# Kernel tuning notes

Measured on AMD Instinct MI355X. Metric: run time of the kernel, lower is better.

## Reference

```python
import jax, jax.numpy as jnp
import numpy as np
from jax import lax

# 4D convolution: XLA's general conv supports 4 spatial dims directly.
# dim numbers: N C + 4 spatial (H1 W1 H2 W2)
_DN = ('NCHWDT', 'OIHWDT', 'NCHWDT')


def conv4d(x, w, b):
    # x: [B, Cin, H1, W1, H2, W2]; w: [Cout, Cin, 3,3,3,3]; b: [Cout]
    y = lax.conv_general_dilated(x, w, window_strides=(1, 1, 1, 1),
                                 padding=[(1, 1)] * 4,
                                 dimension_numbers=_DN)
    return y + b.reshape(1, -1, 1, 1, 1, 1)


def setup_inputs() -> dict:
    key = jax.random.key(0)
    ks = jax.random.split(key, 7)
    B, S = 2, 30
    x = jax.random.normal(ks[0], (B, 1, S, S, S, S), dtype=jnp.float32)
    # Conv4d weights, fan-in scaled (kernel 3^4 = 81)
    w1 = jax.random.normal(ks[1], (10, 1, 3, 3, 3, 3), dtype=jnp.float32) * (1.0 / np.sqrt(1 * 81))
    b1 = jax.random.normal(ks[2], (10,), dtype=jnp.float32) * 0.01
    w2 = jax.random.normal(ks[3], (10, 10, 3, 3, 3, 3), dtype=jnp.float32) * (1.0 / np.sqrt(10 * 81))
    b2 = jax.random.normal(ks[4], (10,), dtype=jnp.float32) * 0.01
    w3 = jax.random.normal(ks[5], (1, 10, 3, 3, 3, 3), dtype=jnp.float32) * (1.0 / np.sqrt(10 * 81))
    b3 = jax.random.normal(ks[6], (1,), dtype=jnp.float32) * 0.01
    return {"x": x, "w1": w1, "b1": b1, "w2": w2, "b2": b2, "w3": w3, "b3": b3}


def reference(x, w1, b1, w2, b2, w3, b3):
    def net(t):
        for w, b in ((w1, b1), (w2, b2), (w3, b3)):
            t = jax.nn.relu(conv4d(t, w, b))
        return t

    # symmetric mode: f(x) + permute(f(permute(x)))
    perm = (0, 1, 4, 5, 2, 3)
    return net(x) + jnp.transpose(net(jnp.transpose(x, perm)), perm)
```

## Files before the change

kernel.cpp:

```cpp
#include <hip/hip_runtime.h>


static constexpr int S  = 30;
static constexpr long S4 = 810000;
static constexpr size_t PLANE = 32768;
static constexpr size_t YBYTES = (size_t)1800 * PLANE;

typedef __bf16 bf16x8 __attribute__((ext_vector_type(8)));
typedef float  f32x16 __attribute__((ext_vector_type(16)));
typedef unsigned int  u32;
typedef unsigned short u16;

static __device__ __forceinline__ u16 f2bf(float f) {
    u32 u = __builtin_bit_cast(u32, f);
    return (u16)((u + 0x7fffu + ((u >> 16) & 1u)) >> 16);
}

__global__ __launch_bounds__(256) void fragprep_k(u32* __restrict__ ft,
    const float* __restrict__ w1, const float* __restrict__ w2,
    const float* __restrict__ w3)
{
    const int gid = blockIdx.x * 256 + threadIdx.x;
    if (gid >= 6 * 27 * 64) return;
    const int lane = gid & 63;
    int r = gid >> 6;
    const int k3 = r % 3; r /= 3;
    const int k12 = r % 9; const int set = r / 9;
    const int layer = set >> 1, swap = set & 1;
    const int k1 = k12 / 3, k2 = k12 % 3;
    const int n = lane & 31, hl = lane >> 5;

    u16 us[8];
#pragma unroll
    for (int j = 0; j < 8; ++j) us[j] = 0;
    if (n < 30) {
        const int k4 = (n < 10) ? 0 : ((n < 20) ? 1 : 2);
        const int co = n - 10 * k4;
        const int i1 = swap ? k3 : k1, i2 = swap ? k4 : k2;
        const int i3 = swap ? k1 : k3, i4 = swap ? k2 : k4;
        const int widx = ((i1 * 3 + i2) * 3 + i3) * 3 + i4;
#pragma unroll
        for (int j = 0; j < 8; ++j) {
            const int k = hl * 8 + j;
            float wv = 0.f;
            if (layer == 0) { if (k == 0) wv = w1[co * 81 + widx]; }
            else if (layer == 1) { if (k < 10) wv = w2[(co * 10 + k) * 81 + widx]; }
            else { if (k < 10 && co == 0) wv = w3[k * 81 + widx]; }
            us[j] = f2bf(wv);
        }
    }
    u32* o = ft + (size_t)gid * 4;
    o[0] = (u32)us[0] | ((u32)us[1] << 16);
    o[1] = (u32)us[2] | ((u32)us[3] << 16);
    o[2] = (u32)us[4] | ((u32)us[5] << 16);
    o[3] = (u32)us[6] | ((u32)us[7] << 16);
}

__global__ __launch_bounds__(128) void zerok(u16* __restrict__ y1, u16* __restrict__ y2)
{
    const int pb = blockIdx.x, tid = threadIdx.x;
    if (tid >= 124) return;
    int hp, tp;
    if (tid < 32)      { hp = 0;        tp = tid; }
    else if (tid < 64) { hp = 31;       tp = tid - 32; }
    else if (tid < 94) { hp = tid - 63; tp = 0; }
    else               { hp = tid - 93; tp = 31; }
    const size_t off = (size_t)pb * PLANE + hp * 1024 + tp * 32;
    const uint4 z = make_uint4(0, 0, 0, 0);
    *(uint4*)((char*)y1 + off)      = z;
    *(uint4*)((char*)y1 + off + 16) = z;
    *(uint4*)((char*)y2 + off)      = z;
    *(uint4*)((char*)y2 + off + 16) = z;
}

template<int LAYER, bool ACCUM>
__global__ __launch_bounds__(256, 2) void conv_k(
    const void* __restrict__ inp, const u32* __restrict__ ftab,
    const float* __restrict__ bias, void* __restrict__ outp)
{
    __shared__ float E[4][1056];
    const int wgid = blockIdx.x + S * blockIdx.y + 900 * blockIdx.z;
    const int id2  = (wgid & 7) * 450 + (wgid >> 3);
    const int half = id2 & 1;
    int sp = id2 >> 1;
    const int w1i = sp % S; sp /= S;
    const int h1  = sp % S;
    const int b   = sp / S;

    const int tid = threadIdx.x;
    const int lane = tid & 63, wv = tid >> 6;
    const int m = lane & 31, hl = lane >> 5;
    const int rbase = half * 15 + wv * 4;
    const uint4* ft4 = (const uint4*)ftab;

    int rofs[6];
#pragma unroll
    for (int f = 0; f < 6; ++f) {
        int rr = rbase + f; if (rr > 31) rr = 31;
        rofs[f] = rr * 1024;
    }

    int kl[9], nk = 0;
#pragma unroll
    for (int k12 = 0; k12 < 9; ++k12) {
        const int g1 = h1 + k12 / 3 - 1, g2 = w1i + k12 % 3 - 1;
        if (g1 >= 0 && g1 < S && g2 >= 0 && g2 < S)
            kl[nk++] = (g1 * S + g2) | (k12 << 10);
    }

    f32x16 acc[4];
#pragma unroll
    for (int r = 0; r < 4; ++r)
#pragma unroll
        for (int e = 0; e < 16; ++e) acc[r][e] = 0.f;

    auto loadA = [&](uint4* Fd, int g) {
        if (LAYER == 0) {
            const float* xp = (const float*)inp + ((size_t)b * 900 + g) * 900;
#pragma unroll
            for (int f = 0; f < 6; ++f) {
                const int hp = rbase + f;
                float v = 0.f;
                if (hl == 0 && hp >= 1 && hp <= 30 && m >= 1 && m <= 30)
                    v = xp[(hp - 1) * 30 + (m - 1)];
                Fd[f] = make_uint4((u32)f2bf(v), 0u, 0u, 0u);
            }
        } else {
            const char* P = (const char*)inp + ((size_t)b * 900 + g) * PLANE
                            + m * 32 + hl * 16;
#pragma unroll
            for (int f = 0; f < 6; ++f)
                Fd[f] = *(const uint4*)(P + rofs[f]);
        }
    };

    uint4 B0[3];
    {
        const int k0 = kl[0] >> 10;
#pragma unroll
        for (int f = 0; f < 3; ++f) B0[f] = ft4[(k0 * 3 + f) * 64 + lane];
    }
    uint4 F[6];
    loadA(F, kl[0] & 1023);

    for (int ki = 0; ki + 1 < nk; ++ki) {
        const int gn = kl[ki + 1] & 1023, kn = kl[ki + 1] >> 10;
        uint4 FN[6];
        loadA(FN, gn);
        uint4 BN[3];
#pragma unroll
        for (int f = 0; f < 3; ++f) BN[f] = ft4[(kn * 3 + f) * 64 + lane];

#pragma unroll
        for (int ss = 0; ss < 3; ++ss)
#pragma unroll
            for (int r = 0; r < 4; ++r)
                acc[r] = __builtin_amdgcn_mfma_f32_32x32x16_bf16(
                    __builtin_bit_cast(bf16x8, F[r + ss]),
                    __builtin_bit_cast(bf16x8, B0[ss]), acc[r], 0, 0, 0);

#pragma unroll
        for (int f = 0; f < 6; ++f) F[f] = FN[f];
#pragma unroll
        for (int f = 0; f < 3; ++f) B0[f] = BN[f];
    }
#pragma unroll
    for (int ss = 0; ss < 3; ++ss)
#pragma unroll
        for (int r = 0; r < 4; ++r)
            acc[r] = __builtin_amdgcn_mfma_f32_32x32x16_bf16(
                __builtin_bit_cast(bf16x8, F[r + ss]),
                __builtin_bit_cast(bf16x8, B0[ss]), acc[r], 0, 0, 0);

    float* Ew = E[wv];
    for (int r = 0; r < 4; ++r) {
        if (wv == 3 && r == 3) continue;
#pragma unroll
        for (int gq = 0; gq < 4; ++gq)
#pragma unroll
            for (int r4 = 0; r4 < 4; ++r4)
                Ew[m * 33 + 4 * hl + 8 * gq + r4] = acc[r][gq * 4 + r4];

        const int h2 = rbase + r;
        if (LAYER <= 1) {
            char* pl = (char*)outp + ((size_t)b * 900 + h1 * S + w1i) * PLANE
                       + (size_t)(h2 + 1) * 1024;
            const int t = lane >> 1, h8 = lane & 1;
            if (t < 30) {
                u32 wo[4];
#pragma unroll
                for (int p = 0; p < 4; ++p) {
                    const int c0 = 8 * h8 + 2 * p, c1 = c0 + 1;
                    float v0 = 0.f, v1 = 0.f;
                    if (c0 < 10)
                        v0 = fmaxf(Ew[c0 * 33 + t] + Ew[(10 + c0) * 33 + t + 1]
                                 + Ew[(20 + c0) * 33 + t + 2] + bias[c0], 0.f);
                    if (c1 < 10)
                        v1 = fmaxf(Ew[c1 * 33 + t] + Ew[(10 + c1) * 33 + t + 1]
                                 + Ew[(20 + c1) * 33 + t + 2] + bias[c1], 0.f);
                    wo[p] = (u32)f2bf(v0) | ((u32)f2bf(v1) << 16);
                }
                *(uint4*)(pl + (t + 1) * 32 + h8 * 16) =
                    make_uint4(wo[0], wo[1], wo[2], wo[3]);
            }
        } else {
            if (lane < 30) {
                const int t = lane;
                float v = Ew[t] + Ew[330 + t + 1] + Ew[660 + t + 2] + bias[0];
                v = fmaxf(v, 0.f);
                float* o = (float*)outp + (size_t)b * S4
                           + (size_t)(h1 * S + w1i) * 900 + h2 * 30 + t;
                if (ACCUM) *o += v; else *o = v;
            }
        }
    }
}

extern "C" void kernel_launch(void* const* d_in, const int* in_sizes, int n_in,
                              void* d_out, int out_size, void* d_ws, size_t ws_size,
                              hipStream_t stream)
{
    const float* x   = (const float*)d_in[0];
    const float* w1p = (const float*)d_in[1];
    const float* b1p = (const float*)d_in[2];
    const float* w2p = (const float*)d_in[3];
    const float* b2p = (const float*)d_in[4];
    const float* w3p = (const float*)d_in[5];
    const float* b3p = (const float*)d_in[6];
    float* out = (float*)d_out;

    u32* ft = (u32*)d_ws;
    u16* y1 = (u16*)((char*)d_ws + 165888);
    u16* y2 = (u16*)((char*)y1 + YBYTES);

    fragprep_k<<<41, 256, 0, stream>>>(ft, w1p, w2p, w3p);
    zerok<<<1800, 128, 0, stream>>>(y1, y2);

    dim3 grid(S, S, 4), blk(256);
    for (int br = 0; br < 2; ++br) {
        const u32* f1 = ft + (size_t)(0 + br) * 27 * 64 * 4;
        const u32* f2 = ft + (size_t)(2 + br) * 27 * 64 * 4;
        const u32* f3 = ft + (size_t)(4 + br) * 27 * 64 * 4;
        conv_k<0, false><<<grid, blk, 0, stream>>>(x,  f1, b1p, (void*)y1);
        conv_k<1, false><<<grid, blk, 0, stream>>>(y1, f2, b2p, (void*)y2);
        if (br == 0)
            conv_k<2, false><<<grid, blk, 0, stream>>>(y2, f3, b3p, (void*)out);
        else
            conv_k<2, true><<<grid, blk, 0, stream>>>(y2, f3, b3p, (void*)out);
    }
}
```

Baseline: 404.4 us.

## Specialize first conv layer to pack nine input planes into one MFMA K-dim

Adds a dedicated layer-0 kernel that packs the 9 (k1,k2) neighbor planes of the single-channel input into the 16-wide bf16 K dimension. This replaces a loop of 9 sparse MFMA passes with one K-slot used. The work drops to 3 MFMA steps per row tile, and all loads are issued up front instead of being software-pipelined. A new fragment table for the packed layer-0 weights is built in fragprep, and the workspace offsets shift to hold it. The kernel also raises the occupancy hint to 4 workgroups per CU.

```diff
diff --git a/kernel.cpp b/kernel.cpp
--- a/kernel.cpp
+++ b/kernel.cpp
@@ -21,32 +21,53 @@
     const float* __restrict__ w3)
 {
     const int gid = blockIdx.x * 256 + threadIdx.x;
-    if (gid >= 6 * 27 * 64) return;
+    if (gid >= 6 * 27 * 64 + 2 * 3 * 64) return;
     const int lane = gid & 63;
-    int r = gid >> 6;
-    const int k3 = r % 3; r /= 3;
-    const int k12 = r % 9; const int set = r / 9;
-    const int layer = set >> 1, swap = set & 1;
-    const int k1 = k12 / 3, k2 = k12 % 3;
     const int n = lane & 31, hl = lane >> 5;
-
     u16 us[8];
 #pragma unroll
     for (int j = 0; j < 8; ++j) us[j] = 0;
-    if (n < 30) {
-        const int k4 = (n < 10) ? 0 : ((n < 20) ? 1 : 2);
-        const int co = n - 10 * k4;
-        const int i1 = swap ? k3 : k1, i2 = swap ? k4 : k2;
-        const int i3 = swap ? k1 : k3, i4 = swap ? k2 : k4;
-        const int widx = ((i1 * 3 + i2) * 3 + i3) * 3 + i4;
-#pragma unroll
-        for (int j = 0; j < 8; ++j) {
-            const int k = hl * 8 + j;
-            float wv = 0.f;
-            if (layer == 0) { if (k == 0) wv = w1[co * 81 + widx]; }
-            else if (layer == 1) { if (k < 10) wv = w2[(co * 10 + k) * 81 + widx]; }
-            else { if (k < 10 && co == 0) wv = w3[k * 81 + widx]; }
-            us[j] = f2bf(wv);
+
+    if (gid < 6 * 27 * 64) {
+        int r = gid >> 6;
+        const int k3 = r % 3; r /= 3;
+        const int k12 = r % 9; const int set = r / 9;
+        const int layer = set >> 1, swap = set & 1;
+        const int k1 = k12 / 3, k2 = k12 % 3;
+        if (n < 30) {
+            const int k4 = (n < 10) ? 0 : ((n < 20) ? 1 : 2);
+            const int co = n - 10 * k4;
+            const int i1 = swap ? k3 : k1, i2 = swap ? k4 : k2;
+            const int i3 = swap ? k1 : k3, i4 = swap ? k2 : k4;
+            const int widx = ((i1 * 3 + i2) * 3 + i3) * 3 + i4;
+#pragma unroll
+            for (int j = 0; j < 8; ++j) {
+                const int k = hl * 8 + j;
+                float wv = 0.f;
+                if (layer == 0) { if (k == 0) wv = w1[co * 81 + widx]; }
+                else if (layer == 1) { if (k < 10) wv = w2[(co * 10 + k) * 81 + widx]; }
+                else { if (k < 10 && co == 0) wv = w3[k * 81 + widx]; }
+                us[j] = f2bf(wv);
+            }
+        }
+    } else {
+        const int idx = gid - 6 * 27 * 64;
+        int r = idx >> 6;
+        const int k3 = r % 3, swap = r / 3;
+        if (n < 30) {
+            const int k4 = (n < 10) ? 0 : ((n < 20) ? 1 : 2);
+            const int co = n - 10 * k4;
+#pragma unroll
+            for (int j = 0; j < 8; ++j) {
+                const int k12 = hl * 8 + j;
+                if (k12 < 9) {
+                    const int k1 = k12 / 3, k2 = k12 % 3;
+                    const int i1 = swap ? k3 : k1, i2 = swap ? k4 : k2;
+                    const int i3 = swap ? k1 : k3, i4 = swap ? k2 : k4;
+                    const int widx = ((i1 * 3 + i2) * 3 + i3) * 3 + i4;
+                    us[j] = f2bf(w1[co * 81 + widx]);
+                }
+            }
         }
     }
     u32* o = ft + (size_t)gid * 4;
@@ -73,9 +94,8 @@
     *(uint4*)((char*)y2 + off + 16) = z;
 }
 
-template<int LAYER, bool ACCUM>
-__global__ __launch_bounds__(256, 2) void conv_k(
-    const void* __restrict__ inp, const u32* __restrict__ ftab,
+__global__ __launch_bounds__(256, 4) void conv0_k(
+    const float* __restrict__ x, const uint4* __restrict__ bt,
     const float* __restrict__ bias, void* __restrict__ outp)
 {
     __shared__ float E[4][1056];
@@ -91,6 +111,113 @@
     const int lane = tid & 63, wv = tid >> 6;
     const int m = lane & 31, hl = lane >> 5;
     const int rbase = half * 15 + wv * 4;
+
+    uint4 Bs[3];
+#pragma unroll
+    for (int ss = 0; ss < 3; ++ss) Bs[ss] = bt[ss * 64 + lane];
+
+    int gof[9]; int gokm = 0;
+#pragma unroll
+    for (int k12 = 0; k12 < 9; ++k12) {
+        const int g1 = h1 + k12 / 3 - 1, g2 = w1i + k12 % 3 - 1;
+        gof[k12] = 0;
+        if (g1 >= 0 && g1 < S && g2 >= 0 && g2 < S) {
+            gof[k12] = (g1 * S + g2) * 900; gokm |= 1 << k12;
+        }
+    }
+    const float* xb = x + (size_t)b * S4;
+
+    uint4 F[6];
+#pragma unroll
+    for (int f = 0; f < 6; ++f) {
+        const int hp = rbase + f;
+        const bool rk = (hp >= 1 && hp <= 30 && m >= 1 && m <= 30);
+        const int ro = (hp - 1) * 30 + (m - 1);
+        u16 av[8];
+#pragma unroll
+        for (int j = 0; j < 8; ++j) av[j] = 0;
+        if (hl == 0) {
+#pragma unroll
+            for (int j = 0; j < 8; ++j) {
+                float v = 0.f;
+                if (rk && ((gokm >> j) & 1)) v = xb[gof[j] + ro];
+                av[j] = f2bf(v);
+            }
+        } else {
+            float v = 0.f;
+            if (rk && ((gokm >> 8) & 1)) v = xb[gof[8] + ro];
+            av[0] = f2bf(v);
+        }
+        F[f] = make_uint4((u32)av[0] | ((u32)av[1] << 16),
+                          (u32)av[2] | ((u32)av[3] << 16),
+                          (u32)av[4] | ((u32)av[5] << 16),
+                          (u32)av[6] | ((u32)av[7] << 16));
+    }
+
+    f32x16 acc[4];
+#pragma unroll
+    for (int r = 0; r < 4; ++r)
+#pragma unroll
+        for (int e = 0; e < 16; ++e) acc[r][e] = 0.f;
+#pragma unroll
+    for (int ss = 0; ss < 3; ++ss)
+#pragma unroll
+        for (int r = 0; r < 4; ++r)
+            acc[r] = __builtin_amdgcn_mfma_f32_32x32x16_bf16(
+                __builtin_bit_cast(bf16x8, F[r + ss]),
+                __builtin_bit_cast(bf16x8, Bs[ss]), acc[r], 0, 0, 0);
+
+    float* Ew = E[wv];
+    for (int r = 0; r < 4; ++r) {
+        if (wv == 3 && r == 3) continue;
+#pragma unroll
+        for (int gq = 0; gq < 4; ++gq)
+#pragma unroll
+            for (int r4 = 0; r4 < 4; ++r4)
+                Ew[m * 33 + 4 * hl + 8 * gq + r4] = acc[r][gq * 4 + r4];
+
+        const int h2 = rbase + r;
+        char* pl = (char*)outp + ((size_t)b * 900 + h1 * S + w1i) * PLANE
+                   + (size_t)(h2 + 1) * 1024;
+        const int t = lane >> 1, h8 = lane & 1;
+        if (t < 30) {
+            u32 wo[4];
+#pragma unroll
+            for (int p = 0; p < 4; ++p) {
+                const int c0 = 8 * h8 + 2 * p, c1 = c0 + 1;
+                float v0 = 0.f, v1 = 0.f;
+                if (c0 < 10)
+                    v0 = fmaxf(Ew[c0 * 33 + t] + Ew[(10 + c0) * 33 + t + 1]
+                             + Ew[(20 + c0) * 33 + t + 2] + bias[c0], 0.f);
+                if (c1 < 10)
+                    v1 = fmaxf(Ew[c1 * 33 + t] + Ew[(10 + c1) * 33 + t + 1]
+                             + Ew[(20 + c1) * 33 + t + 2] + bias[c1], 0.f);
+                wo[p] = (u32)f2bf(v0) | ((u32)f2bf(v1) << 16);
+            }
+            *(uint4*)(pl + (t + 1) * 32 + h8 * 16) =
+                make_uint4(wo[0], wo[1], wo[2], wo[3]);
+        }
+    }
+}
+
+template<int LAYER, bool ACCUM>
+__global__ __launch_bounds__(256, 2) void conv_k(
+    const void* __restrict__ inp, const u32* __restrict__ ftab,
+    const float* __restrict__ bias, void* __restrict__ outp)
+{
+    __shared__ float E[4][1056];
+    const int wgid = blockIdx.x + S * blockIdx.y + 900 * blockIdx.z;
+    const int id2  = (wgid & 7) * 450 + (wgid >> 3);
+    const int half = id2 & 1;
+    int sp = id2 >> 1;
+    const int w1i = sp % S; sp /= S;
+    const int h1  = sp % S;
+    const int b   = sp / S;
+
+    const int tid = threadIdx.x;
+    const int lane = tid & 63, wv = tid >> 6;
+    const int m = lane & 31, hl = lane >> 5;
+    const int rbase = half * 15 + wv * 4;
     const uint4* ft4 = (const uint4*)ftab;
 
     int rofs[6];
@@ -115,23 +242,11 @@
         for (int e = 0; e < 16; ++e) acc[r][e] = 0.f;
 
     auto loadA = [&](uint4* Fd, int g) {
-        if (LAYER == 0) {
-            const float* xp = (const float*)inp + ((size_t)b * 900 + g) * 900;
-#pragma unroll
-            for (int f = 0; f < 6; ++f) {
-                const int hp = rbase + f;
-                float v = 0.f;
-                if (hl == 0 && hp >= 1 && hp <= 30 && m >= 1 && m <= 30)
-                    v = xp[(hp - 1) * 30 + (m - 1)];
-                Fd[f] = make_uint4((u32)f2bf(v), 0u, 0u, 0u);
-            }
-        } else {
-            const char* P = (const char*)inp + ((size_t)b * 900 + g) * PLANE
-                            + m * 32 + hl * 16;
-#pragma unroll
-            for (int f = 0; f < 6; ++f)
-                Fd[f] = *(const uint4*)(P + rofs[f]);
-        }
+        const char* P = (const char*)inp + ((size_t)b * 900 + g) * PLANE
+                        + m * 32 + hl * 16;
+#pragma unroll
+        for (int f = 0; f < 6; ++f)
+            Fd[f] = *(const uint4*)(P + rofs[f]);
     };
 
     uint4 B0[3];
@@ -230,18 +345,18 @@
     float* out = (float*)d_out;
 
     u32* ft = (u32*)d_ws;
-    u16* y1 = (u16*)((char*)d_ws + 165888);
+    const uint4* ftL0 = (const uint4*)d_ws + 6 * 27 * 64;
+    u16* y1 = (u16*)((char*)d_ws + 172032);
     u16* y2 = (u16*)((char*)y1 + YBYTES);
 
-    fragprep_k<<<41, 256, 0, stream>>>(ft, w1p, w2p, w3p);
+    fragprep_k<<<42, 256, 0, stream>>>(ft, w1p, w2p, w3p);
     zerok<<<1800, 128, 0, stream>>>(y1, y2);
 
     dim3 grid(S, S, 4), blk(256);
     for (int br = 0; br < 2; ++br) {
-        const u32* f1 = ft + (size_t)(0 + br) * 27 * 64 * 4;
         const u32* f2 = ft + (size_t)(2 + br) * 27 * 64 * 4;
         const u32* f3 = ft + (size_t)(4 + br) * 27 * 64 * 4;
-        conv_k<0, false><<<grid, blk, 0, stream>>>(x,  f1, b1p, (void*)y1);
+        conv0_k<<<grid, blk, 0, stream>>>(x, ftL0 + br * 192, b1p, (void*)y1);
         conv_k<1, false><<<grid, blk, 0, stream>>>(y1, f2, b2p, (void*)y2);
         if (br == 0)
             conv_k<2, false><<<grid, blk, 0, stream>>>(y2, f3, b3p, (void*)out);
```

Result: no change. 396.9 us (-1.8%).
